# Performance work log

Measured on AMD Instinct MI355X. Metric: run time of the kernel, lower is better.

## Reference

```python
import jax, jax.numpy as jnp
import numpy as np

ALPHA = 0.3      # robust Welsch scale (hardcoded in calc_chamfer)
EPS = 1e-6       # cosine_similarity eps


def _single_direction(x_points, x_normals, y_points, y_normals):
    """Robust chamfer x->y with K=1 KNN. Returns (mean robust dist, mean normal loss)."""
    # brute-force squared pairwise distances: [B, N, M]
    x2 = jnp.sum(x_points * x_points, axis=-1)            # [B, N]
    y2 = jnp.sum(y_points * y_points, axis=-1)            # [B, M]
    d2 = x2[:, :, None] + y2[:, None, :] - 2.0 * jnp.einsum('bnd,bmd->bnm', x_points, y_points)
    d2 = jnp.maximum(d2, 0.0)
    idx = jnp.argmin(d2, axis=-1)                         # [B, N] nearest neighbor in y
    dists = jnp.take_along_axis(d2, idx[..., None], axis=-1)[..., 0]   # squared dists [B, N]
    # Welsch weight applied to the squared distance (matches torch code), detached
    w = jax.lax.stop_gradient(jnp.exp(-(dists ** 2) / (2.0 * ALPHA * ALPHA)))
    cham_x = jnp.sum(w * dists, axis=1)                   # [B]
    # gather nearest normals and cosine similarity (torch-style per-vector eps clamp)
    yn_near = jnp.take_along_axis(y_normals, idx[..., None], axis=1)   # [B, N, 3]
    xn_norm = jnp.maximum(jnp.linalg.norm(x_normals, axis=-1), EPS)
    yn_norm = jnp.maximum(jnp.linalg.norm(yn_near, axis=-1), EPS)
    cos = jnp.sum(x_normals * yn_near, axis=-1) / (xn_norm * yn_norm)
    cham_norm_x = 1.0 - jnp.abs(cos)                      # abs_cosine=True
    return jnp.mean(cham_x), jnp.mean(cham_norm_x)


def setup_inputs() -> dict:
    key = jax.random.key(0)
    k1, k2, k3, k4 = jax.random.split(key, 4)
    B, N, M = 2, 10000, 10000
    pred_points = jax.random.normal(k1, (B, N, 3), dtype=jnp.float32)
    target_points = jax.random.normal(k2, (B, M, 3), dtype=jnp.float32)
    pn = jax.random.normal(k3, (B, N, 3), dtype=jnp.float32)
    tn = jax.random.normal(k4, (B, M, 3), dtype=jnp.float32)
    pred_normals = pn / jnp.linalg.norm(pn, axis=-1, keepdims=True)
    target_normals = tn / jnp.linalg.norm(tn, axis=-1, keepdims=True)
    return {
        'pred_points': pred_points,
        'pred_normals': pred_normals,
        'target_points': target_points,
        'target_normals': target_normals,
    }


def reference(pred_points, pred_normals, target_points, target_normals):
    # direction 1: target -> pred, direction 2: pred -> target
    d1, n1 = _single_direction(target_points, target_normals, pred_points, pred_normals)
    d2, n2 = _single_direction(pred_points, pred_normals, target_points, target_normals)
    return (d1 + d2, n1 + n2)
```

## Files before the change

kernel.cpp:

```cpp
#include <hip/hip_runtime.h>
#include <math.h>

#define NPTS 10000
#define XPT 8
#define AXCH 5
#define TILE 500

__global__ __launch_bounds__(256) void knn_max(
    const float* __restrict__ pred_pts, const float* __restrict__ targ_pts,
    float* __restrict__ wsM, int nslices)
{
    const int slice = NPTS / nslices;
    const int c   = blockIdx.z;
    const int dir = c >> 1, b = c & 1;
    const float* xp = (dir == 0 ? targ_pts : pred_pts) + (size_t)b * NPTS * 3;
    const float* yp = (dir == 0 ? pred_pts : targ_pts) + (size_t)b * NPTS * 3;
    const int s = blockIdx.y;
    const int base = blockIdx.x * (256 * XPT) + threadIdx.x;

    __shared__ float4 sy[TILE];

    float xx[XPT][3];
#pragma unroll
    for (int k = 0; k < XPT; ++k) {
        const int n = base + k * 256;
        const int nn = (n < NPTS) ? n : (NPTS - 1);
        xx[k][0] = xp[nn * 3 + 0];
        xx[k][1] = xp[nn * 3 + 1];
        xx[k][2] = xp[nn * 3 + 2];
    }
    float best[XPT];
#pragma unroll
    for (int k = 0; k < XPT; ++k) best[k] = -1e30f;

    const int jstart = s * slice, jend = jstart + slice;
    for (int t0 = jstart; t0 < jend; t0 += TILE) {
        const int cnt = min(TILE, jend - t0);
        __syncthreads();
        for (int j = threadIdx.x; j < cnt; j += 256) {
            const float a  = yp[(t0 + j) * 3 + 0];
            const float bb = yp[(t0 + j) * 3 + 1];
            const float cc = yp[(t0 + j) * 3 + 2];
            sy[j] = make_float4(a, bb, cc, -0.5f * (a * a + bb * bb + cc * cc));
        }
        __syncthreads();
#pragma unroll 4
        for (int j = 0; j < cnt; j += 2) {
            const float4 ya = sy[j];
            const float4 yb = sy[j + 1];
#pragma unroll
            for (int k = 0; k < XPT; ++k) {
                const float ma = fmaf(xx[k][0], ya.x,
                                 fmaf(xx[k][1], ya.y,
                                 fmaf(xx[k][2], ya.z, ya.w)));
                const float mb = fmaf(xx[k][0], yb.x,
                                 fmaf(xx[k][1], yb.y,
                                 fmaf(xx[k][2], yb.z, yb.w)));
                best[k] = fmaxf(fmaxf(best[k], ma), mb);
            }
        }
    }
#pragma unroll
    for (int k = 0; k < XPT; ++k) {
        const int n = base + k * 256;
        if (n < NPTS)
            wsM[((size_t)(c * nslices + s)) * NPTS + n] = best[k];
    }
}

__global__ __launch_bounds__(256) void finalize(
    const float* __restrict__ pred_pts, const float* __restrict__ pred_nrm,
    const float* __restrict__ targ_pts, const float* __restrict__ targ_nrm,
    const float* __restrict__ wsM, float2* __restrict__ wsB, int nslices)
{
    const int c   = blockIdx.y;
    const int dir = c >> 1, b = c & 1;
    const float* xp = (dir == 0 ? targ_pts : pred_pts) + (size_t)b * NPTS * 3;
    const float* xn = (dir == 0 ? targ_nrm : pred_nrm) + (size_t)b * NPTS * 3;
    const float* yp = (dir == 0 ? pred_pts : targ_pts) + (size_t)b * NPTS * 3;
    const float* yn = (dir == 0 ? pred_nrm : targ_nrm) + (size_t)b * NPTS * 3;

    const int lane = threadIdx.x & 7;
    const int n = blockIdx.x * 32 + (threadIdx.x >> 3);

    float t0 = 0.f, t1 = 0.f;
    if (n < NPTS) {
        float bm = -1e30f;
        int   bs = 1 << 30;
        for (int s = lane; s < nslices; s += 8) {
            const float m = wsM[((size_t)(c * nslices + s)) * NPTS + n];
            if (m > bm) { bm = m; bs = s; }
        }
#pragma unroll
        for (int w = 1; w < 8; w <<= 1) {
            const float mo = __shfl_xor(bm, w);
            const int   so = __shfl_xor(bs, w);
            if (mo > bm || (mo == bm && so < bs)) { bm = mo; bs = so; }
        }
        const float a  = xp[n * 3 + 0];
        const float bb = xp[n * 3 + 1];
        const float cc = xp[n * 3 + 2];
        const int slice = NPTS / nslices;
        const int j0 = bs * slice;
        float rb = -1e30f;
        int bidx = 1 << 30;
        for (int j = j0 + lane; j < j0 + slice; j += 8) {
            const float ya = yp[j * 3 + 0];
            const float yb = yp[j * 3 + 1];
            const float yc = yp[j * 3 + 2];
            const float hy = -0.5f * (ya * ya + yb * yb + yc * yc);
            const float m  = fmaf(a, ya, fmaf(bb, yb, fmaf(cc, yc, hy)));
            if (m > rb) { rb = m; bidx = j; }
        }
#pragma unroll
        for (int w = 1; w < 8; w <<= 1) {
            const float mo = __shfl_xor(rb, w);
            const int   jo = __shfl_xor(bidx, w);
            if (mo > rb || (mo == rb && jo < bidx)) { rb = mo; bidx = jo; }
        }
        if (lane == 0) {
            const float hx = -0.5f * (a * a + bb * bb + cc * cc);
            float d2 = -2.0f * (rb + hx);
            d2 = fmaxf(d2, 0.0f);
            const float w = __expf(-(d2 * d2) * (1.0f / 0.18f));
            t0 = w * d2;
            const float nx0 = xn[n * 3 + 0], nx1 = xn[n * 3 + 1], nx2 = xn[n * 3 + 2];
            const float ny0 = yn[(size_t)bidx * 3 + 0];
            const float ny1 = yn[(size_t)bidx * 3 + 1];
            const float ny2 = yn[(size_t)bidx * 3 + 2];
            const float nnx = fmaxf(sqrtf(nx0 * nx0 + nx1 * nx1 + nx2 * nx2), 1e-6f);
            const float nny = fmaxf(sqrtf(ny0 * ny0 + ny1 * ny1 + ny2 * ny2), 1e-6f);
            const float cosv = (nx0 * ny0 + nx1 * ny1 + nx2 * ny2) / (nnx * nny);
            t1 = 1.0f - fabsf(cosv);
        }
    }

    __shared__ float r0[256], r1[256];
    r0[threadIdx.x] = t0;
    r1[threadIdx.x] = t1;
    __syncthreads();
    for (int st = 128; st > 0; st >>= 1) {
        if (threadIdx.x < st) {
            r0[threadIdx.x] += r0[threadIdx.x + st];
            r1[threadIdx.x] += r1[threadIdx.x + st];
        }
        __syncthreads();
    }
    if (threadIdx.x == 0)
        wsB[blockIdx.y * gridDim.x + blockIdx.x] = make_float2(r0[0], r1[0]);
}

__global__ __launch_bounds__(256) void reduce_final(
    const float2* __restrict__ wsB, int nblocks, float* __restrict__ out)
{
    __shared__ float r0[256], r1[256];
    const int t = threadIdx.x;
    float s0 = 0.f, s1 = 0.f;
    for (int i = t; i < nblocks; i += 256) {
        const float2 v = wsB[i];
        s0 += v.x;
        s1 += v.y;
    }
    r0[t] = s0; r1[t] = s1;
    __syncthreads();
    for (int st = 128; st > 0; st >>= 1) {
        if (t < st) { r0[t] += r0[t + st]; r1[t] += r1[t + st]; }
        __syncthreads();
    }
    if (t == 0) {
        out[0] = 0.5f * r0[0];
        out[1] = r1[0] * (1.0f / 20000.0f);
    }
}

extern "C" void kernel_launch(void* const* d_in, const int* in_sizes, int n_in,
                              void* d_out, int out_size, void* d_ws, size_t ws_size,
                              hipStream_t stream)
{
    const float* pred_pts = (const float*)d_in[0];
    const float* pred_nrm = (const float*)d_in[1];
    const float* targ_pts = (const float*)d_in[2];
    const float* targ_nrm = (const float*)d_in[3];
    float* out = (float*)d_out;

    const int BXCH = (NPTS + 31) / 32;

    const int ladder[5] = {40, 20, 10, 5, 2};
    int ns = 2;
    for (int i = 0; i < 5; ++i) {
        const size_t need = (size_t)4 * ladder[i] * NPTS * sizeof(float)
                          + (size_t)4 * BXCH * sizeof(float2) + 256;
        if (need <= ws_size) { ns = ladder[i]; break; }
    }

    float*  wsM = (float*)d_ws;
    float2* wsB = (float2*)(wsM + (size_t)4 * ns * NPTS);

    dim3 gA(AXCH, ns, 4);
    knn_max<<<gA, 256, 0, stream>>>(pred_pts, targ_pts, wsM, ns);

    dim3 gB(BXCH, 4);
    finalize<<<gB, 256, 0, stream>>>(pred_pts, pred_nrm, targ_pts, targ_nrm,
                                     wsM, wsB, ns);

    reduce_final<<<1, 256, 0, stream>>>(wsB, BXCH * 4, out);
}
```

Baseline: 56.81 us.

## Use packed FP32 FMA for half the query points and repack shared tile

Reorganizes the shared-memory target tile into pairs of points so that two candidate distances can be computed with v_pk_fma_f32 inline assembly for four of the eight query points per thread. The other four use scalar FMAs on the same packed layout, presumably to keep both issue paths busy. It also adds a launch-bounds occupancy hint and raises the slice-count ladder, which gives more blocks but larger finalize scans. Packed FMA halves the instruction count for part of the work, but it relies on inline asm the compiler cannot schedule and assumes an even slice size.

```diff
diff --git a/kernel.cpp b/kernel.cpp
--- a/kernel.cpp
+++ b/kernel.cpp
@@ -6,7 +6,12 @@
 #define AXCH 5
 #define TILE 500
 
-__global__ __launch_bounds__(256) void knn_max(
+typedef float float2v __attribute__((ext_vector_type(2)));
+
+#define PKFMA(d, a, b, c) \
+    asm("v_pk_fma_f32 %0, %1, %2, %3" : "=v"(d) : "v"(a), "v"(b), "v"(c))
+
+__global__ __launch_bounds__(256, 4) void knn_max(
     const float* __restrict__ pred_pts, const float* __restrict__ targ_pts,
     float* __restrict__ wsM, int nslices)
 {
@@ -18,50 +23,70 @@
     const int s = blockIdx.y;
     const int base = blockIdx.x * (256 * XPT) + threadIdx.x;
 
-    __shared__ float4 sy[TILE];
-
-    float xx[XPT][3];
-#pragma unroll
-    for (int k = 0; k < XPT; ++k) {
+    __shared__ float4 spk[TILE];
+
+    float2v xb[4][3];
+    float   xs[4][3];
+#pragma unroll
+    for (int k = 0; k < 8; ++k) {
         const int n = base + k * 256;
         const int nn = (n < NPTS) ? n : (NPTS - 1);
-        xx[k][0] = xp[nn * 3 + 0];
-        xx[k][1] = xp[nn * 3 + 1];
-        xx[k][2] = xp[nn * 3 + 2];
-    }
-    float best[XPT];
-#pragma unroll
-    for (int k = 0; k < XPT; ++k) best[k] = -1e30f;
+        const float v0 = xp[nn * 3 + 0];
+        const float v1 = xp[nn * 3 + 1];
+        const float v2 = xp[nn * 3 + 2];
+        if (k < 4) {
+            xb[k][0] = (float2v){v0, v0};
+            xb[k][1] = (float2v){v1, v1};
+            xb[k][2] = (float2v){v2, v2};
+        } else {
+            xs[k - 4][0] = v0; xs[k - 4][1] = v1; xs[k - 4][2] = v2;
+        }
+    }
+    float best[8];
+#pragma unroll
+    for (int k = 0; k < 8; ++k) best[k] = -1e30f;
 
     const int jstart = s * slice, jend = jstart + slice;
     for (int t0 = jstart; t0 < jend; t0 += TILE) {
         const int cnt = min(TILE, jend - t0);
-        __syncthreads();
-        for (int j = threadIdx.x; j < cnt; j += 256) {
-            const float a  = yp[(t0 + j) * 3 + 0];
-            const float bb = yp[(t0 + j) * 3 + 1];
-            const float cc = yp[(t0 + j) * 3 + 2];
-            sy[j] = make_float4(a, bb, cc, -0.5f * (a * a + bb * bb + cc * cc));
-        }
-        __syncthreads();
-#pragma unroll 4
-        for (int j = 0; j < cnt; j += 2) {
-            const float4 ya = sy[j];
-            const float4 yb = sy[j + 1];
-#pragma unroll
-            for (int k = 0; k < XPT; ++k) {
-                const float ma = fmaf(xx[k][0], ya.x,
-                                 fmaf(xx[k][1], ya.y,
-                                 fmaf(xx[k][2], ya.z, ya.w)));
-                const float mb = fmaf(xx[k][0], yb.x,
-                                 fmaf(xx[k][1], yb.y,
-                                 fmaf(xx[k][2], yb.z, yb.w)));
-                best[k] = fmaxf(fmaxf(best[k], ma), mb);
+        const int np  = cnt >> 1;
+        __syncthreads();
+        for (int p = threadIdx.x; p < np; p += 256) {
+            const int j = t0 + 2 * p;
+            const float a0 = yp[j * 3 + 0], b0 = yp[j * 3 + 1], c0 = yp[j * 3 + 2];
+            const float a1 = yp[j * 3 + 3], b1 = yp[j * 3 + 4], c1 = yp[j * 3 + 5];
+            spk[2 * p]     = make_float4(a0, a1, b0, b1);
+            spk[2 * p + 1] = make_float4(c0, c1,
+                                         -0.5f * (a0 * a0 + b0 * b0 + c0 * c0),
+                                         -0.5f * (a1 * a1 + b1 * b1 + c1 * c1));
+        }
+        __syncthreads();
+#pragma unroll 2
+        for (int p = 0; p < np; ++p) {
+            const float4 A = spk[2 * p];
+            const float4 B = spk[2 * p + 1];
+            const float2v px = {A.x, A.y}, py = {A.z, A.w};
+            const float2v pz = {B.x, B.y}, pw = {B.z, B.w};
+#pragma unroll
+            for (int k = 0; k < 4; ++k) {
+                float2v t;
+                PKFMA(t, xb[k][2], pz, pw);
+                PKFMA(t, xb[k][1], py, t);
+                PKFMA(t, xb[k][0], px, t);
+                best[k] = fmaxf(fmaxf(best[k], t.x), t.y);
             }
-        }
-    }
-#pragma unroll
-    for (int k = 0; k < XPT; ++k) {
+#pragma unroll
+            for (int k = 0; k < 4; ++k) {
+                const float ma = fmaf(xs[k][0], A.x,
+                                 fmaf(xs[k][1], A.z, fmaf(xs[k][2], B.x, B.z)));
+                const float mb = fmaf(xs[k][0], A.y,
+                                 fmaf(xs[k][1], A.w, fmaf(xs[k][2], B.y, B.w)));
+                best[4 + k] = fmaxf(fmaxf(best[4 + k], ma), mb);
+            }
+        }
+    }
+#pragma unroll
+    for (int k = 0; k < 8; ++k) {
         const int n = base + k * 256;
         if (n < NPTS)
             wsM[((size_t)(c * nslices + s)) * NPTS + n] = best[k];
@@ -185,9 +210,9 @@
 
     const int BXCH = (NPTS + 31) / 32;
 
-    const int ladder[5] = {40, 20, 10, 5, 2};
-    int ns = 2;
-    for (int i = 0; i < 5; ++i) {
+    const int ladder[4] = {50, 40, 25, 10};
+    int ns = 10;
+    for (int i = 0; i < 4; ++i) {
         const size_t need = (size_t)4 * ladder[i] * NPTS * sizeof(float)
                           + (size_t)4 * BXCH * sizeof(float2) + 256;
         if (need <= ws_size) { ns = ladder[i]; break; }
```

After: 54.89 us. -3.4%, faster.

## Prepack y points to float4 and stream from global instead of LDS tiles

Applied to the files above, without the earlier changes.

Adds a pack kernel that writes each candidate point as a float4 holding xyz and minus half its squared norm. The KNN kernel then drops its shared-memory tiling and syncthreads and reads these uniform float4s straight from global/L1. The finalize refinement reads the same packed data. XPT is halved and x-blocks doubled, the slice ladder tops out at 20, and launch bounds request 4 blocks per SM. The aim is to remove LDS staging and barrier cost and raise occupancy, at the price of an extra launch and workspace, with reuse now relying on the cache.

```diff
diff --git a/kernel.cpp b/kernel.cpp
--- a/kernel.cpp
+++ b/kernel.cpp
@@ -2,23 +2,36 @@
 #include <math.h>
 
 #define NPTS 10000
-#define XPT 8
-#define AXCH 5
-#define TILE 500
-
-__global__ __launch_bounds__(256) void knn_max(
+#define XPT 4
+#define AXCH 10
+
+__global__ __launch_bounds__(256) void pack_y(
     const float* __restrict__ pred_pts, const float* __restrict__ targ_pts,
-    float* __restrict__ wsM, int nslices)
+    float4* __restrict__ y4)
+{
+    const int idx = blockIdx.x * 256 + threadIdx.x;
+    if (idx >= 4 * NPTS) return;
+    const int c = idx / NPTS;
+    const int j = idx - c * NPTS;
+    const int dir = c >> 1, b = c & 1;
+    const float* yp = (dir == 0 ? pred_pts : targ_pts) + (size_t)b * NPTS * 3;
+    const float a  = yp[j * 3 + 0];
+    const float bb = yp[j * 3 + 1];
+    const float cc = yp[j * 3 + 2];
+    y4[idx] = make_float4(a, bb, cc, -0.5f * (a * a + bb * bb + cc * cc));
+}
+
+__global__ __launch_bounds__(256, 4) void knn_max(
+    const float* __restrict__ pred_pts, const float* __restrict__ targ_pts,
+    const float4* __restrict__ y4, float* __restrict__ wsM, int nslices)
 {
     const int slice = NPTS / nslices;
     const int c   = blockIdx.z;
     const int dir = c >> 1, b = c & 1;
     const float* xp = (dir == 0 ? targ_pts : pred_pts) + (size_t)b * NPTS * 3;
-    const float* yp = (dir == 0 ? pred_pts : targ_pts) + (size_t)b * NPTS * 3;
+    const float4* __restrict__ yq = y4 + (size_t)c * NPTS;
     const int s = blockIdx.y;
     const int base = blockIdx.x * (256 * XPT) + threadIdx.x;
-
-    __shared__ float4 sy[TILE];
 
     float xx[XPT][3];
 #pragma unroll
@@ -33,31 +46,20 @@
 #pragma unroll
     for (int k = 0; k < XPT; ++k) best[k] = -1e30f;
 
-    const int jstart = s * slice, jend = jstart + slice;
-    for (int t0 = jstart; t0 < jend; t0 += TILE) {
-        const int cnt = min(TILE, jend - t0);
-        __syncthreads();
-        for (int j = threadIdx.x; j < cnt; j += 256) {
-            const float a  = yp[(t0 + j) * 3 + 0];
-            const float bb = yp[(t0 + j) * 3 + 1];
-            const float cc = yp[(t0 + j) * 3 + 2];
-            sy[j] = make_float4(a, bb, cc, -0.5f * (a * a + bb * bb + cc * cc));
-        }
-        __syncthreads();
+    const int js = s * slice, je = js + slice;
 #pragma unroll 4
-        for (int j = 0; j < cnt; j += 2) {
-            const float4 ya = sy[j];
-            const float4 yb = sy[j + 1];
-#pragma unroll
-            for (int k = 0; k < XPT; ++k) {
-                const float ma = fmaf(xx[k][0], ya.x,
-                                 fmaf(xx[k][1], ya.y,
-                                 fmaf(xx[k][2], ya.z, ya.w)));
-                const float mb = fmaf(xx[k][0], yb.x,
-                                 fmaf(xx[k][1], yb.y,
-                                 fmaf(xx[k][2], yb.z, yb.w)));
-                best[k] = fmaxf(fmaxf(best[k], ma), mb);
-            }
+    for (int j = js; j < je; j += 2) {
+        const float4 Y0 = yq[j];
+        const float4 Y1 = yq[j + 1];
+#pragma unroll
+        for (int k = 0; k < XPT; ++k) {
+            const float ma = fmaf(xx[k][0], Y0.x,
+                             fmaf(xx[k][1], Y0.y,
+                             fmaf(xx[k][2], Y0.z, Y0.w)));
+            const float mb = fmaf(xx[k][0], Y1.x,
+                             fmaf(xx[k][1], Y1.y,
+                             fmaf(xx[k][2], Y1.z, Y1.w)));
+            best[k] = fmaxf(fmaxf(best[k], ma), mb);
         }
     }
 #pragma unroll
@@ -71,14 +73,15 @@
 __global__ __launch_bounds__(256) void finalize(
     const float* __restrict__ pred_pts, const float* __restrict__ pred_nrm,
     const float* __restrict__ targ_pts, const float* __restrict__ targ_nrm,
-    const float* __restrict__ wsM, float2* __restrict__ wsB, int nslices)
+    const float4* __restrict__ y4, const float* __restrict__ wsM,
+    float2* __restrict__ wsB, int nslices)
 {
     const int c   = blockIdx.y;
     const int dir = c >> 1, b = c & 1;
     const float* xp = (dir == 0 ? targ_pts : pred_pts) + (size_t)b * NPTS * 3;
     const float* xn = (dir == 0 ? targ_nrm : pred_nrm) + (size_t)b * NPTS * 3;
-    const float* yp = (dir == 0 ? pred_pts : targ_pts) + (size_t)b * NPTS * 3;
     const float* yn = (dir == 0 ? pred_nrm : targ_nrm) + (size_t)b * NPTS * 3;
+    const float4* __restrict__ yq = y4 + (size_t)c * NPTS;
 
     const int lane = threadIdx.x & 7;
     const int n = blockIdx.x * 32 + (threadIdx.x >> 3);
@@ -105,11 +108,8 @@
         float rb = -1e30f;
         int bidx = 1 << 30;
         for (int j = j0 + lane; j < j0 + slice; j += 8) {
-            const float ya = yp[j * 3 + 0];
-            const float yb = yp[j * 3 + 1];
-            const float yc = yp[j * 3 + 2];
-            const float hy = -0.5f * (ya * ya + yb * yb + yc * yc);
-            const float m  = fmaf(a, ya, fmaf(bb, yb, fmaf(cc, yc, hy)));
+            const float4 Y = yq[j];
+            const float m = fmaf(a, Y.x, fmaf(bb, Y.y, fmaf(cc, Y.z, Y.w)));
             if (m > rb) { rb = m; bidx = j; }
         }
 #pragma unroll
@@ -184,24 +184,28 @@
     float* out = (float*)d_out;
 
     const int BXCH = (NPTS + 31) / 32;
-
-    const int ladder[5] = {40, 20, 10, 5, 2};
+    const size_t Y4B = (size_t)4 * NPTS * sizeof(float4);
+
+    const int ladder[5] = {20, 10, 5, 4, 2};
     int ns = 2;
     for (int i = 0; i < 5; ++i) {
-        const size_t need = (size_t)4 * ladder[i] * NPTS * sizeof(float)
+        const size_t need = Y4B + (size_t)4 * ladder[i] * NPTS * sizeof(float)
                           + (size_t)4 * BXCH * sizeof(float2) + 256;
         if (need <= ws_size) { ns = ladder[i]; break; }
     }
 
-    float*  wsM = (float*)d_ws;
+    float4* y4  = (float4*)d_ws;
+    float*  wsM = (float*)((char*)d_ws + Y4B);
     float2* wsB = (float2*)(wsM + (size_t)4 * ns * NPTS);
 
+    pack_y<<<(4 * NPTS + 255) / 256, 256, 0, stream>>>(pred_pts, targ_pts, y4);
+
     dim3 gA(AXCH, ns, 4);
-    knn_max<<<gA, 256, 0, stream>>>(pred_pts, targ_pts, wsM, ns);
+    knn_max<<<gA, 256, 0, stream>>>(pred_pts, targ_pts, y4, wsM, ns);
 
     dim3 gB(BXCH, 4);
     finalize<<<gB, 256, 0, stream>>>(pred_pts, pred_nrm, targ_pts, targ_nrm,
-                                     wsM, wsB, ns);
+                                     y4, wsM, wsB, ns);
 
     reduce_final<<<1, 256, 0, stream>>>(wsB, BXCH * 4, out);
 }
```

After: 86.79 us. 52.8% more time.

## Quantize per-slice maxima to 16-bit and rescan all tied slices per point

Applied to the files above, without the earlier changes.

The KNN pass now uses a fixed 50 slices of 200 points, each loaded once into shared memory. Each per-slice maximum is stored as a 16-bit quantized code in point-major layout rather than as a float, which cuts workspace traffic. Finalize gives one 64-lane wave to each point: it reads all slice codes, finds the maximum code, and rescans every slice whose code ties it, so quantization cannot drop the true nearest neighbour. In exchange, finalize may rescan several slices and the workspace size is now hardcoded with no fallback ladder.

```diff
diff --git a/kernel.cpp b/kernel.cpp
--- a/kernel.cpp
+++ b/kernel.cpp
@@ -4,13 +4,19 @@
 #define NPTS 10000
 #define XPT 8
 #define AXCH 5
-#define TILE 500
-
-__global__ __launch_bounds__(256) void knn_max(
+#define NS 50
+#define SLICE 200
+
+__device__ __forceinline__ unsigned short enc_q(float m) {
+    int q = (int)floorf((m + 32.0f) * 1024.0f);
+    q = q < 0 ? 0 : (q > 65535 ? 65535 : q);
+    return (unsigned short)q;
+}
+
+__global__ __launch_bounds__(256, 4) void knn_max(
     const float* __restrict__ pred_pts, const float* __restrict__ targ_pts,
-    float* __restrict__ wsM, int nslices)
-{
-    const int slice = NPTS / nslices;
+    unsigned short* __restrict__ wsQ)
+{
     const int c   = blockIdx.z;
     const int dir = c >> 1, b = c & 1;
     const float* xp = (dir == 0 ? targ_pts : pred_pts) + (size_t)b * NPTS * 3;
@@ -18,7 +24,7 @@
     const int s = blockIdx.y;
     const int base = blockIdx.x * (256 * XPT) + threadIdx.x;
 
-    __shared__ float4 sy[TILE];
+    __shared__ float4 sy[SLICE];
 
     float xx[XPT][3];
 #pragma unroll
@@ -33,45 +39,43 @@
 #pragma unroll
     for (int k = 0; k < XPT; ++k) best[k] = -1e30f;
 
-    const int jstart = s * slice, jend = jstart + slice;
-    for (int t0 = jstart; t0 < jend; t0 += TILE) {
-        const int cnt = min(TILE, jend - t0);
-        __syncthreads();
-        for (int j = threadIdx.x; j < cnt; j += 256) {
-            const float a  = yp[(t0 + j) * 3 + 0];
-            const float bb = yp[(t0 + j) * 3 + 1];
-            const float cc = yp[(t0 + j) * 3 + 2];
-            sy[j] = make_float4(a, bb, cc, -0.5f * (a * a + bb * bb + cc * cc));
+    const int js = s * SLICE;
+    for (int j = threadIdx.x; j < SLICE; j += 256) {
+        const float a  = yp[(js + j) * 3 + 0];
+        const float bb = yp[(js + j) * 3 + 1];
+        const float cc = yp[(js + j) * 3 + 2];
+        sy[j] = make_float4(a, bb, cc, -0.5f * fmaf(cc, cc, fmaf(bb, bb, a * a)));
+    }
+    __syncthreads();
+
+#pragma unroll 4
+    for (int j = 0; j < SLICE; j += 2) {
+        const float4 Y0 = sy[j];
+        const float4 Y1 = sy[j + 1];
+#pragma unroll
+        for (int k = 0; k < XPT; ++k) {
+            const float ma = fmaf(xx[k][0], Y0.x,
+                             fmaf(xx[k][1], Y0.y,
+                             fmaf(xx[k][2], Y0.z, Y0.w)));
+            const float mb = fmaf(xx[k][0], Y1.x,
+                             fmaf(xx[k][1], Y1.y,
+                             fmaf(xx[k][2], Y1.z, Y1.w)));
+            best[k] = fmaxf(fmaxf(best[k], ma), mb);
         }
-        __syncthreads();
-#pragma unroll 4
-        for (int j = 0; j < cnt; j += 2) {
-            const float4 ya = sy[j];
-            const float4 yb = sy[j + 1];
-#pragma unroll
-            for (int k = 0; k < XPT; ++k) {
-                const float ma = fmaf(xx[k][0], ya.x,
-                                 fmaf(xx[k][1], ya.y,
-                                 fmaf(xx[k][2], ya.z, ya.w)));
-                const float mb = fmaf(xx[k][0], yb.x,
-                                 fmaf(xx[k][1], yb.y,
-                                 fmaf(xx[k][2], yb.z, yb.w)));
-                best[k] = fmaxf(fmaxf(best[k], ma), mb);
-            }
-        }
-    }
+    }
+
 #pragma unroll
     for (int k = 0; k < XPT; ++k) {
         const int n = base + k * 256;
         if (n < NPTS)
-            wsM[((size_t)(c * nslices + s)) * NPTS + n] = best[k];
-    }
-}
-
-__global__ __launch_bounds__(256) void finalize(
+            wsQ[((size_t)c * NPTS + n) * NS + s] = enc_q(best[k]);
+    }
+}
+
+__global__ __launch_bounds__(512) void finalize(
     const float* __restrict__ pred_pts, const float* __restrict__ pred_nrm,
     const float* __restrict__ targ_pts, const float* __restrict__ targ_nrm,
-    const float* __restrict__ wsM, float2* __restrict__ wsB, int nslices)
+    const unsigned short* __restrict__ wsQ, float2* __restrict__ wsB)
 {
     const int c   = blockIdx.y;
     const int dir = c >> 1, b = c & 1;
@@ -80,66 +84,65 @@
     const float* yp = (dir == 0 ? pred_pts : targ_pts) + (size_t)b * NPTS * 3;
     const float* yn = (dir == 0 ? pred_nrm : targ_nrm) + (size_t)b * NPTS * 3;
 
-    const int lane = threadIdx.x & 7;
-    const int n = blockIdx.x * 32 + (threadIdx.x >> 3);
+    const int lane = threadIdx.x & 63;
+    const int wv   = threadIdx.x >> 6;
+    const int n    = blockIdx.x * 8 + wv;
+
+    int q = -1;
+    if (lane < NS) q = wsQ[((size_t)c * NPTS + n) * NS + lane];
+    int qmax = q;
+#pragma unroll
+    for (int w = 1; w < 64; w <<= 1)
+        qmax = max(qmax, __shfl_xor(qmax, w));
+
+    const float a  = xp[n * 3 + 0];
+    const float bb = xp[n * 3 + 1];
+    const float cc = xp[n * 3 + 2];
+
+    float rb = -1e30f;
+    int bidx = 1 << 30;
+    for (int s = 0; s < NS; ++s) {
+        if (__shfl(q, s) == qmax) {
+            const int jend = (s + 1) * SLICE;
+            for (int j = s * SLICE + lane; j < jend; j += 64) {
+                const float ya = yp[j * 3 + 0];
+                const float yb = yp[j * 3 + 1];
+                const float yc = yp[j * 3 + 2];
+                const float hy = -0.5f * fmaf(yc, yc, fmaf(yb, yb, ya * ya));
+                const float m  = fmaf(a, ya, fmaf(bb, yb, fmaf(cc, yc, hy)));
+                if (m > rb) { rb = m; bidx = j; }
+            }
+        }
+    }
+#pragma unroll
+    for (int w = 1; w < 64; w <<= 1) {
+        const float mo = __shfl_xor(rb, w);
+        const int   jo = __shfl_xor(bidx, w);
+        if (mo > rb || (mo == rb && jo < bidx)) { rb = mo; bidx = jo; }
+    }
 
     float t0 = 0.f, t1 = 0.f;
-    if (n < NPTS) {
-        float bm = -1e30f;
-        int   bs = 1 << 30;
-        for (int s = lane; s < nslices; s += 8) {
-            const float m = wsM[((size_t)(c * nslices + s)) * NPTS + n];
-            if (m > bm) { bm = m; bs = s; }
-        }
-#pragma unroll
-        for (int w = 1; w < 8; w <<= 1) {
-            const float mo = __shfl_xor(bm, w);
-            const int   so = __shfl_xor(bs, w);
-            if (mo > bm || (mo == bm && so < bs)) { bm = mo; bs = so; }
-        }
-        const float a  = xp[n * 3 + 0];
-        const float bb = xp[n * 3 + 1];
-        const float cc = xp[n * 3 + 2];
-        const int slice = NPTS / nslices;
-        const int j0 = bs * slice;
-        float rb = -1e30f;
-        int bidx = 1 << 30;
-        for (int j = j0 + lane; j < j0 + slice; j += 8) {
-            const float ya = yp[j * 3 + 0];
-            const float yb = yp[j * 3 + 1];
-            const float yc = yp[j * 3 + 2];
-            const float hy = -0.5f * (ya * ya + yb * yb + yc * yc);
-            const float m  = fmaf(a, ya, fmaf(bb, yb, fmaf(cc, yc, hy)));
-            if (m > rb) { rb = m; bidx = j; }
-        }
-#pragma unroll
-        for (int w = 1; w < 8; w <<= 1) {
-            const float mo = __shfl_xor(rb, w);
-            const int   jo = __shfl_xor(bidx, w);
-            if (mo > rb || (mo == rb && jo < bidx)) { rb = mo; bidx = jo; }
-        }
-        if (lane == 0) {
-            const float hx = -0.5f * (a * a + bb * bb + cc * cc);
-            float d2 = -2.0f * (rb + hx);
-            d2 = fmaxf(d2, 0.0f);
-            const float w = __expf(-(d2 * d2) * (1.0f / 0.18f));
-            t0 = w * d2;
-            const float nx0 = xn[n * 3 + 0], nx1 = xn[n * 3 + 1], nx2 = xn[n * 3 + 2];
-            const float ny0 = yn[(size_t)bidx * 3 + 0];
-            const float ny1 = yn[(size_t)bidx * 3 + 1];
-            const float ny2 = yn[(size_t)bidx * 3 + 2];
-            const float nnx = fmaxf(sqrtf(nx0 * nx0 + nx1 * nx1 + nx2 * nx2), 1e-6f);
-            const float nny = fmaxf(sqrtf(ny0 * ny0 + ny1 * ny1 + ny2 * ny2), 1e-6f);
-            const float cosv = (nx0 * ny0 + nx1 * ny1 + nx2 * ny2) / (nnx * nny);
-            t1 = 1.0f - fabsf(cosv);
-        }
-    }
-
-    __shared__ float r0[256], r1[256];
+    if (lane == 0) {
+        const float hx = -0.5f * fmaf(cc, cc, fmaf(bb, bb, a * a));
+        float d2 = -2.0f * (rb + hx);
+        d2 = fmaxf(d2, 0.0f);
+        const float w = __expf(-(d2 * d2) * (1.0f / 0.18f));
+        t0 = w * d2;
+        const float nx0 = xn[n * 3 + 0], nx1 = xn[n * 3 + 1], nx2 = xn[n * 3 + 2];
+        const float ny0 = yn[(size_t)bidx * 3 + 0];
+        const float ny1 = yn[(size_t)bidx * 3 + 1];
+        const float ny2 = yn[(size_t)bidx * 3 + 2];
+        const float nnx = fmaxf(sqrtf(nx0 * nx0 + nx1 * nx1 + nx2 * nx2), 1e-6f);
+        const float nny = fmaxf(sqrtf(ny0 * ny0 + ny1 * ny1 + ny2 * ny2), 1e-6f);
+        const float cosv = (nx0 * ny0 + nx1 * ny1 + nx2 * ny2) / (nnx * nny);
+        t1 = 1.0f - fabsf(cosv);
+    }
+
+    __shared__ float r0[512], r1[512];
     r0[threadIdx.x] = t0;
     r1[threadIdx.x] = t1;
     __syncthreads();
-    for (int st = 128; st > 0; st >>= 1) {
+    for (int st = 256; st > 0; st >>= 1) {
         if (threadIdx.x < st) {
             r0[threadIdx.x] += r0[threadIdx.x + st];
             r1[threadIdx.x] += r1[threadIdx.x + st];
@@ -183,25 +186,17 @@
     const float* targ_nrm = (const float*)d_in[3];
     float* out = (float*)d_out;
 
-    const int BXCH = (NPTS + 31) / 32;
-
-    const int ladder[5] = {40, 20, 10, 5, 2};
-    int ns = 2;
-    for (int i = 0; i < 5; ++i) {
-        const size_t need = (size_t)4 * ladder[i] * NPTS * sizeof(float)
-                          + (size_t)4 * BXCH * sizeof(float2) + 256;
-        if (need <= ws_size) { ns = ladder[i]; break; }
-    }
-
-    float*  wsM = (float*)d_ws;
-    float2* wsB = (float2*)(wsM + (size_t)4 * ns * NPTS);
-
-    dim3 gA(AXCH, ns, 4);
-    knn_max<<<gA, 256, 0, stream>>>(pred_pts, targ_pts, wsM, ns);
+    const int BXCH = NPTS / 8;
+
+    unsigned short* wsQ = (unsigned short*)d_ws;
+    float2* wsB = (float2*)((char*)d_ws + (size_t)4 * NPTS * NS * sizeof(unsigned short));
+
+    dim3 gA(AXCH, NS, 4);
+    knn_max<<<gA, 256, 0, stream>>>(pred_pts, targ_pts, wsQ);
 
     dim3 gB(BXCH, 4);
-    finalize<<<gB, 256, 0, stream>>>(pred_pts, pred_nrm, targ_pts, targ_nrm,
-                                     wsM, wsB, ns);
+    finalize<<<gB, 512, 0, stream>>>(pred_pts, pred_nrm, targ_pts, targ_nrm,
+                                     wsQ, wsB);
 
     reduce_final<<<1, 256, 0, stream>>>(wsB, BXCH * 4, out);
 }
```

After: 89.60 us. +57.7%, slower.
